# Kernel optimization log

Measured on AMD Instinct MI355X. Metric: run time of the kernel, lower is better.

Reference implementation:

```python
import jax, jax.numpy as jnp
import numpy as np

HIDDEN = 1024
STATE = 256
EXP = 4
LN_EPS = 1e-5


def setup_inputs() -> dict:
    key = jax.random.key(0)
    ks = jax.random.split(key, 10)
    B, T, H, S = 8, 2048, HIDDEN, STATE
    x = jax.random.normal(ks[0], (B, T, H), dtype=jnp.float32)
    A = jax.random.normal(ks[1], (S, S), dtype=jnp.float32) * 0.1
    Bm = jax.random.normal(ks[2], (S, H), dtype=jnp.float32) * 0.1
    C = jax.random.normal(ks[3], (H, S), dtype=jnp.float32) * 0.1
    D = jax.random.normal(ks[4], (H, H), dtype=jnp.float32) * 0.1
    ln_w = jnp.ones((H,), dtype=jnp.float32)
    ln_b = jnp.zeros((H,), dtype=jnp.float32)
    lim1 = 1.0 / np.sqrt(H)
    lim2 = 1.0 / np.sqrt(H * EXP)
    W1 = jax.random.uniform(ks[5], (H * EXP, H), minval=-lim1, maxval=lim1, dtype=jnp.float32)
    b1 = jax.random.uniform(ks[6], (H * EXP,), minval=-lim1, maxval=lim1, dtype=jnp.float32)
    W2 = jax.random.uniform(ks[7], (H, H * EXP), minval=-lim2, maxval=lim2, dtype=jnp.float32)
    b2 = jax.random.uniform(ks[8], (H,), minval=-lim2, maxval=lim2, dtype=jnp.float32)
    return {"x": x, "A": A, "Bm": Bm, "C": C, "D": D,
            "ln_w": ln_w, "ln_b": ln_b, "W1": W1, "b1": b1, "W2": W2, "b2": b2}


def _layernorm(y, w, b):
    mu = jnp.mean(y, axis=-1, keepdims=True)
    var = jnp.var(y, axis=-1, keepdims=True)
    return (y - mu) * jax.lax.rsqrt(var + LN_EPS) * w + b


def reference(x, A, Bm, C, D, ln_w, ln_b, W1, b1, W2, b2):
    Bsz, T, H = x.shape
    S = A.shape[0]
    state0 = jnp.zeros((Bsz, S), dtype=x.dtype)
    # Precompute input projections for all timesteps (big GEMMs outside the scan)
    xB = jnp.einsum('bth,sh->tbs', x, Bm)   # [T,B,S]
    xD = jnp.einsum('bth,oh->tbo', x, D)    # [T,B,H]

    def step(state, inp):
        xb_t, xd_t = inp
        state = jnp.tanh(state @ A.T + xb_t)
        out = state @ C.T + xd_t
        return state, out

    final_state, outs = jax.lax.scan(step, state0, (xB, xD))
    out_seq = jnp.transpose(outs, (1, 0, 2))  # [B,T,H]
    y = _layernorm(out_seq + x, ln_w, ln_b)
    # FFN (dropout is identity in eval mode); torch GELU default = exact erf
    h = jax.nn.gelu(jnp.einsum('bth,fh->btf', y, W1) + b1, approximate=False)
    y = y + jnp.einsum('btf,hf->bth', h, W2) + b2
    return (y, final_state)
```

## Files before the change

kernel.cpp:

```cpp
#include <hip/hip_runtime.h>
#include <math.h>

typedef unsigned short u16;
typedef unsigned int u32;

using short8 = __attribute__((ext_vector_type(8))) short;
using f32x4  = __attribute__((ext_vector_type(4))) float;
typedef _Float16 h2_t __attribute__((ext_vector_type(2)));

typedef const __attribute__((address_space(1))) unsigned int* gas_ptr;
typedef __attribute__((address_space(3))) unsigned int* las_ptr;

__device__ __forceinline__ void load_lds16(const void* g, void* l) {
    __builtin_amdgcn_global_load_lds((gas_ptr)g, (las_ptr)l, 16, 0, 0);
}

__device__ __forceinline__ u16 bf16b(float f) {
    u32 u = __builtin_bit_cast(u32, f);
    u += 0x7fffu + ((u >> 16) & 1u);
    return (u16)(u >> 16);
}
__device__ __forceinline__ float b2f(u16 h) {
    u32 u = (u32)h << 16;
    return __builtin_bit_cast(float, u);
}

__global__ void cvt_kernel(const float4* __restrict__ s, ushort4* __restrict__ d, int n4) {
    for (int i = blockIdx.x * blockDim.x + threadIdx.x; i < n4; i += gridDim.x * blockDim.x) {
        float4 v = s[i];
        ushort4 o;
        o.x = bf16b(v.x); o.y = bf16b(v.y); o.z = bf16b(v.z); o.w = bf16b(v.w);
        d[i] = o;
    }
}

template<int MODE>
__global__ __launch_bounds__(256) void gemm_bf16(
    const u16* __restrict__ Ab, const u16* __restrict__ Bb, int K, int ktiles,
    float* __restrict__ out32, u16* __restrict__ out16,
    const float* __restrict__ bias, const float* __restrict__ addf,
    const u16* __restrict__ add16, int out_stride, int out_col0)
{
    __shared__ __align__(16) u16 Als[128 * 64];
    __shared__ __align__(16) u16 Bls[128 * 64];

    const int tid  = threadIdx.x;
    const int lane = tid & 63;
    const int w    = tid >> 6;
    const int wr   = (w >> 1) * 64;
    const int wc   = (w & 1) * 64;
    const int fr   = lane & 15;
    const int fkB  = (lane >> 4) * 16;

    const size_t rb = (size_t)K * 2;
    const char* Ag = (const char*)Ab + ((size_t)blockIdx.y * 128 + (tid >> 3)) * rb + (size_t)(tid & 7) * 16;
    const char* Bg = (const char*)Bb + ((size_t)blockIdx.x * 128 + (tid >> 3)) * rb + (size_t)(tid & 7) * 16;
    char* Ald = (char*)Als + tid * 16;
    char* Bld = (char*)Bls + tid * 16;

    f32x4 acc[4][4];
#pragma unroll
    for (int m = 0; m < 4; ++m)
#pragma unroll
        for (int n = 0; n < 4; ++n)
            acc[m][n] = f32x4{0.f, 0.f, 0.f, 0.f};

    for (int kt = 0; kt < ktiles; ++kt) {
        __syncthreads();
        const char* Asrc = Ag + (size_t)kt * 128;
        const char* Bsrc = Bg + (size_t)kt * 128;
#pragma unroll
        for (int i = 0; i < 4; ++i) {
            load_lds16(Asrc + (size_t)(i * 32) * rb, Ald + i * 4096);
            load_lds16(Bsrc + (size_t)(i * 32) * rb, Bld + i * 4096);
        }
        __syncthreads();
#pragma unroll
        for (int kk = 0; kk < 2; ++kk) {
            short8 af[4], bfr[4];
#pragma unroll
            for (int m = 0; m < 4; ++m)
                af[m] = *(const short8*)((const char*)Als + (wr + m * 16 + fr) * 128 + kk * 64 + fkB);
#pragma unroll
            for (int n = 0; n < 4; ++n)
                bfr[n] = *(const short8*)((const char*)Bls + (wc + n * 16 + fr) * 128 + kk * 64 + fkB);
#pragma unroll
            for (int m = 0; m < 4; ++m)
#pragma unroll
                for (int n = 0; n < 4; ++n)
                    acc[m][n] = __builtin_amdgcn_mfma_f32_16x16x32_bf16(af[m], bfr[n], acc[m][n], 0, 0, 0);
        }
    }

    const int rbase = blockIdx.y * 128 + wr + (lane >> 4) * 4;
    const int cbase = blockIdx.x * 128 + wc + fr;
#pragma unroll
    for (int m = 0; m < 4; ++m) {
#pragma unroll
        for (int n = 0; n < 4; ++n) {
            const int col = cbase + n * 16;
#pragma unroll
            for (int r = 0; r < 4; ++r) {
                const int row = rbase + m * 16 + r;
                float v = acc[m][n][r];
                if (MODE == 0) {
                    out16[(size_t)row * out_stride + out_col0 + col] = bf16b(v);
                } else if (MODE == 1) {
                    out32[(size_t)row * 1024 + col] =
                        v + addf[(size_t)row * 1024 + col] + b2f(add16[(size_t)row * 1280 + 256 + col]);
                } else if (MODE == 2) {
                    float u = v + bias[col];
                    u = 0.5f * u * (1.0f + erff(u * 0.70710678118654752f));
                    out16[(size_t)row * out_stride + col] = bf16b(u);
                } else {
                    out32[(size_t)row * 1024 + col] =
                        v + bias[col] + b2f(add16[(size_t)row * 1024 + col]);
                }
            }
        }
    }
}

__global__ __launch_bounds__(512) void scan_kernel(
    const float* __restrict__ Am, const u16* __restrict__ xBb ,
    u16* __restrict__ states, float* __restrict__ fstate)
{
    __shared__ __align__(16) u32 stp[128];
    const int tid  = threadIdx.x;
    const int b    = blockIdx.x;
    const int s    = tid >> 1;
    const int half = tid & 1;

    h2_t a[64];
    {
        const float4* ar = (const float4*)(Am + s * 256 + half * 128);
#pragma unroll
        for (int j = 0; j < 32; ++j) {
            float4 f = ar[j];
            a[2 * j]     = h2_t{(_Float16)f.x, (_Float16)f.y};
            a[2 * j + 1] = h2_t{(_Float16)f.z, (_Float16)f.w};
        }
    }
    if (tid < 128) stp[tid] = 0u;
    const u16* xrow = xBb + (size_t)b * 2048 * 1280 + s;
    u16* srow = states + (size_t)b * 2048 * 256 + s;

    float xb0 = b2f(xrow[0]);
    float xb1 = b2f(xrow[1280]);
    float xb2 = b2f(xrow[2 * 1280]);
    float xb3 = b2f(xrow[3 * 1280]);
    __syncthreads();

#define SCAN_STEP(T, XB, NEXT)                                                      \
    {                                                                               \
        float acc = 0.f;                                                            \
        const u32* sp = stp + half * 64;                                            \
        _Pragma("unroll")                                                           \
        for (int j = 0; j < 16; ++j) {                                              \
            uint4 sv = *(const uint4*)(sp + 4 * j);                                 \
            acc = __builtin_amdgcn_fdot2(a[4 * j + 0], __builtin_bit_cast(h2_t, sv.x), acc, false); \
            acc = __builtin_amdgcn_fdot2(a[4 * j + 1], __builtin_bit_cast(h2_t, sv.y), acc, false); \
            acc = __builtin_amdgcn_fdot2(a[4 * j + 2], __builtin_bit_cast(h2_t, sv.z), acc, false); \
            acc = __builtin_amdgcn_fdot2(a[4 * j + 3], __builtin_bit_cast(h2_t, sv.w), acc, false); \
        }                                                                           \
        float z = acc + __shfl_xor(acc, 1) + (XB);                                  \
        int tp = (T) + 4 <= 2047 ? (T) + 4 : 2047;                                  \
        (XB) = b2f(xrow[(size_t)tp * 1280]);                                        \
        float e = __expf(2.f * z);                                                  \
        float h = 1.f - 2.f / (e + 1.f);                                            \
        __syncthreads();                                                            \
        if (!half) {                                                                \
            reinterpret_cast<_Float16*>(stp)[s] = (_Float16)h;                      \
            srow[(size_t)(T) * 256] = bf16b(h);                                     \
            if ((T) == 2047) fstate[b * 256 + s] = h;                               \
        }                                                                           \
        __syncthreads();                                                            \
    }

    for (int t = 0; t < 2048; t += 4) {
        SCAN_STEP(t + 0, xb0, );
        SCAN_STEP(t + 1, xb1, );
        SCAN_STEP(t + 2, xb2, );
        SCAN_STEP(t + 3, xb3, );
    }
#undef SCAN_STEP
}

__global__ __launch_bounds__(256) void ln_kernel(
    const float* __restrict__ pre , const float* __restrict__ gam,
    const float* __restrict__ bet, u16* __restrict__ ybf)
{
    const int row = blockIdx.x, tid = threadIdx.x;
    const float4 v = *(const float4*)(pre + (size_t)row * 1024 + tid * 4);
    float sum = v.x + v.y + v.z + v.w;
    float sq  = v.x * v.x + v.y * v.y + v.z * v.z + v.w * v.w;
#pragma unroll
    for (int o = 32; o; o >>= 1) { sum += __shfl_xor(sum, o); sq += __shfl_xor(sq, o); }
    __shared__ float red[8];
    const int lane = tid & 63, wv = tid >> 6;
    if (!lane) { red[wv] = sum; red[4 + wv] = sq; }
    __syncthreads();
    sum = red[0] + red[1] + red[2] + red[3];
    sq  = red[4] + red[5] + red[6] + red[7];
    const float mu  = sum * (1.f / 1024.f);
    const float var = sq * (1.f / 1024.f) - mu * mu;
    const float rs  = rsqrtf(var + 1e-5f);
    const float4 g  = *(const float4*)(gam + tid * 4);
    const float4 be = *(const float4*)(bet + tid * 4);
    ushort4 ob;
    ob.x = bf16b((v.x - mu) * rs * g.x + be.x);
    ob.y = bf16b((v.y - mu) * rs * g.y + be.y);
    ob.z = bf16b((v.z - mu) * rs * g.z + be.z);
    ob.w = bf16b((v.w - mu) * rs * g.w + be.w);
    *(ushort4*)(ybf + (size_t)row * 1024 + tid * 4) = ob;
}

extern "C" void kernel_launch(void* const* d_in, const int* in_sizes, int n_in,
                              void* d_out, int out_size, void* d_ws, size_t ws_size,
                              hipStream_t stream)
{
    const float* x    = (const float*)d_in[0];
    const float* A    = (const float*)d_in[1];
    const float* Bm   = (const float*)d_in[2];
    const float* C    = (const float*)d_in[3];
    const float* D    = (const float*)d_in[4];
    const float* ln_w = (const float*)d_in[5];
    const float* ln_b = (const float*)d_in[6];
    const float* W1   = (const float*)d_in[7];
    const float* b1   = (const float*)d_in[8];
    const float* W2   = (const float*)d_in[9];
    const float* b2   = (const float*)d_in[10];

    char* ws = (char*)d_ws;
    u16*   BmD    = (u16*)(ws + 0);
    u16*   C_bf   = (u16*)(ws + 2621440);
    u16*   W1b    = (u16*)(ws + 3145728);
    u16*   W2b    = (u16*)(ws + 11534336);
    u16*   xBD_bf = (u16*)(ws + 19922944);
    u16*   st_bf  = (u16*)(ws + 61865984);
    u16*   y_bf   = (u16*)(ws + 70254592);
    u16*   h_bf   = (u16*)(ws + 103809024);

    float* out  = (float*)d_out;
    u16*   x_bf = (u16*)d_out;

    cvt_kernel<<<2048, 256, 0, stream>>>((const float4*)x,  (ushort4*)x_bf, 4194304);
    cvt_kernel<<<256,  256, 0, stream>>>((const float4*)Bm, (ushort4*)BmD, 65536);
    cvt_kernel<<<1024, 256, 0, stream>>>((const float4*)D,  (ushort4*)(BmD + 262144), 262144);
    cvt_kernel<<<256,  256, 0, stream>>>((const float4*)C,  (ushort4*)C_bf, 65536);
    cvt_kernel<<<2048, 256, 0, stream>>>((const float4*)W1, (ushort4*)W1b, 1048576);
    cvt_kernel<<<2048, 256, 0, stream>>>((const float4*)W2, (ushort4*)W2b, 1048576);

    dim3 blk(256);
    gemm_bf16<0><<<dim3(10, 128), blk, 0, stream>>>(x_bf, BmD, 1024, 16,
        nullptr, xBD_bf, nullptr, nullptr, nullptr, 1280, 0);
    scan_kernel<<<8, 512, 0, stream>>>(A, xBD_bf, st_bf, out + 16777216);
    gemm_bf16<1><<<dim3(8, 128), blk, 0, stream>>>(st_bf, C_bf, 256, 4,
        out, nullptr, nullptr, x, xBD_bf, 1024, 0);
    ln_kernel<<<16384, 256, 0, stream>>>(out, ln_w, ln_b, y_bf);
    for (int c = 0; c < 4; ++c) {
        const u16* yc = y_bf + (size_t)c * 4096 * 1024;
        float* oc = out + (size_t)c * 4096 * 1024;
        gemm_bf16<2><<<dim3(32, 32), blk, 0, stream>>>(yc, W1b, 1024, 16,
            nullptr, h_bf, b1, nullptr, nullptr, 4096, 0);
        gemm_bf16<3><<<dim3(8, 32), blk, 0, stream>>>(h_bf, W2b, 4096, 64,
            oc, nullptr, b2, nullptr, yc, 1024, 0);
    }
}
```

Measured before the change: 2.311 ms.

## Fold D projection into state-output GEMM and widen scan to 1024 threads

```diff
diff --git a/kernel.cpp b/kernel.cpp
--- a/kernel.cpp
+++ b/kernel.cpp
@@ -33,13 +33,24 @@
         d[i] = o;
     }
 }
+__global__ void cvt_str_kernel(const float4* __restrict__ s, u16* __restrict__ d,
+                               int K4, int n4, int stride, int col0) {
+    for (int i = blockIdx.x * blockDim.x + threadIdx.x; i < n4; i += gridDim.x * blockDim.x) {
+        float4 v = s[i];
+        int r = i / K4, k4 = (i - r * K4) * 4;
+        ushort4 o;
+        o.x = bf16b(v.x); o.y = bf16b(v.y); o.z = bf16b(v.z); o.w = bf16b(v.w);
+        *(ushort4*)(d + (size_t)r * stride + col0 + k4) = o;
+    }
+}
 
 template<int MODE>
 __global__ __launch_bounds__(256) void gemm_bf16(
-    const u16* __restrict__ Ab, const u16* __restrict__ Bb, int K, int ktiles,
+    const u16* __restrict__ Ab, const u16* __restrict__ Ab2, const u16* __restrict__ Bb,
+    int K, int ktiles,
     float* __restrict__ out32, u16* __restrict__ out16,
     const float* __restrict__ bias, const float* __restrict__ addf,
-    const u16* __restrict__ add16, int out_stride, int out_col0)
+    const u16* __restrict__ add16, int out_stride)
 {
     __shared__ __align__(16) u16 Als[128 * 64];
     __shared__ __align__(16) u16 Bls[128 * 64];
@@ -52,9 +63,11 @@
     const int fr   = lane & 15;
     const int fkB  = (lane >> 4) * 16;
 
-    const size_t rb = (size_t)K * 2;
-    const char* Ag = (const char*)Ab + ((size_t)blockIdx.y * 128 + (tid >> 3)) * rb + (size_t)(tid & 7) * 16;
-    const char* Bg = (const char*)Bb + ((size_t)blockIdx.x * 128 + (tid >> 3)) * rb + (size_t)(tid & 7) * 16;
+    const size_t rbB = (size_t)K * 2;
+    const int arow = blockIdx.y * 128 + (tid >> 3);
+    const char* Ag  = (const char*)Ab + (size_t)arow * ((MODE == 1) ? 512 : rbB) + (size_t)(tid & 7) * 16;
+    const char* Ag2 = (MODE == 1) ? ((const char*)Ab2 + (size_t)arow * 2048 + (size_t)(tid & 7) * 16) : nullptr;
+    const char* Bg  = (const char*)Bb + ((size_t)blockIdx.x * 128 + (tid >> 3)) * rbB + (size_t)(tid & 7) * 16;
     char* Ald = (char*)Als + tid * 16;
     char* Bld = (char*)Bls + tid * 16;
 
@@ -67,12 +80,19 @@
 
     for (int kt = 0; kt < ktiles; ++kt) {
         __syncthreads();
-        const char* Asrc = Ag + (size_t)kt * 128;
+        const char* Asrc;
+        size_t rbA;
+        if (MODE == 1) {
+            if (kt < 4) { Asrc = Ag  + (size_t)kt * 128;       rbA = 512;  }
+            else        { Asrc = Ag2 + (size_t)(kt - 4) * 128; rbA = 2048; }
+        } else {
+            Asrc = Ag + (size_t)kt * 128; rbA = rbB;
+        }
         const char* Bsrc = Bg + (size_t)kt * 128;
 #pragma unroll
         for (int i = 0; i < 4; ++i) {
-            load_lds16(Asrc + (size_t)(i * 32) * rb, Ald + i * 4096);
-            load_lds16(Bsrc + (size_t)(i * 32) * rb, Bld + i * 4096);
+            load_lds16(Asrc + (size_t)(i * 32) * rbA, Ald + i * 4096);
+            load_lds16(Bsrc + (size_t)(i * 32) * rbB, Bld + i * 4096);
         }
         __syncthreads();
 #pragma unroll
@@ -104,10 +124,9 @@
                 const int row = rbase + m * 16 + r;
                 float v = acc[m][n][r];
                 if (MODE == 0) {
-                    out16[(size_t)row * out_stride + out_col0 + col] = bf16b(v);
+                    out16[(size_t)row * out_stride + col] = bf16b(v);
                 } else if (MODE == 1) {
-                    out32[(size_t)row * 1024 + col] =
-                        v + addf[(size_t)row * 1024 + col] + b2f(add16[(size_t)row * 1280 + 256 + col]);
+                    out16[(size_t)row * 1024 + col] = bf16b(v + addf[(size_t)row * 1024 + col]);
                 } else if (MODE == 2) {
                     float u = v + bias[col];
                     u = 0.5f * u * (1.0f + erff(u * 0.70710678118654752f));
@@ -121,56 +140,59 @@
     }
 }
 
-__global__ __launch_bounds__(512) void scan_kernel(
+__global__ __launch_bounds__(1024) void scan_kernel(
     const float* __restrict__ Am, const u16* __restrict__ xBb ,
     u16* __restrict__ states, float* __restrict__ fstate)
 {
-    __shared__ __align__(16) u32 stp[128];
-    const int tid  = threadIdx.x;
-    const int b    = blockIdx.x;
-    const int s    = tid >> 1;
-    const int half = tid & 1;
-
-    h2_t a[64];
+    __shared__ __align__(16) u32 SB[2][144];
+    const int tid = threadIdx.x;
+    const int b   = blockIdx.x;
+    const int s   = tid >> 2;
+    const int q   = tid & 3;
+
+    h2_t a[32];
     {
-        const float4* ar = (const float4*)(Am + s * 256 + half * 128);
-#pragma unroll
-        for (int j = 0; j < 32; ++j) {
+        const float4* ar = (const float4*)(Am + s * 256 + q * 64);
+#pragma unroll
+        for (int j = 0; j < 16; ++j) {
             float4 f = ar[j];
             a[2 * j]     = h2_t{(_Float16)f.x, (_Float16)f.y};
             a[2 * j + 1] = h2_t{(_Float16)f.z, (_Float16)f.w};
         }
     }
-    if (tid < 128) stp[tid] = 0u;
-    const u16* xrow = xBb + (size_t)b * 2048 * 1280 + s;
+    if (tid < 144) SB[0][tid] = 0u;
+
+    const u16* xrow = xBb + (size_t)b * 2048 * 256 + s;
     u16* srow = states + (size_t)b * 2048 * 256 + s;
+    const int widx = (s >> 6) * 72 + (s & 63);
 
     float xb0 = b2f(xrow[0]);
-    float xb1 = b2f(xrow[1280]);
-    float xb2 = b2f(xrow[2 * 1280]);
-    float xb3 = b2f(xrow[3 * 1280]);
+    float xb1 = b2f(xrow[256]);
+    float xb2 = b2f(xrow[512]);
+    float xb3 = b2f(xrow[768]);
     __syncthreads();
 
-#define SCAN_STEP(T, XB, NEXT)                                                      \
+#define SCAN_STEP(T, XB)                                                            \
     {                                                                               \
-        float acc = 0.f;                                                            \
-        const u32* sp = stp + half * 64;                                            \
+        const u32* sp = SB[(T) & 1] + q * 36;                                       \
+        float ac0 = 0.f, ac1 = 0.f, ac2 = 0.f, ac3 = 0.f;                           \
         _Pragma("unroll")                                                           \
-        for (int j = 0; j < 16; ++j) {                                              \
+        for (int j = 0; j < 8; ++j) {                                               \
             uint4 sv = *(const uint4*)(sp + 4 * j);                                 \
-            acc = __builtin_amdgcn_fdot2(a[4 * j + 0], __builtin_bit_cast(h2_t, sv.x), acc, false); \
-            acc = __builtin_amdgcn_fdot2(a[4 * j + 1], __builtin_bit_cast(h2_t, sv.y), acc, false); \
-            acc = __builtin_amdgcn_fdot2(a[4 * j + 2], __builtin_bit_cast(h2_t, sv.z), acc, false); \
-            acc = __builtin_amdgcn_fdot2(a[4 * j + 3], __builtin_bit_cast(h2_t, sv.w), acc, false); \
+            ac0 = __builtin_amdgcn_fdot2(a[4 * j + 0], __builtin_bit_cast(h2_t, sv.x), ac0, false); \
+            ac1 = __builtin_amdgcn_fdot2(a[4 * j + 1], __builtin_bit_cast(h2_t, sv.y), ac1, false); \
+            ac2 = __builtin_amdgcn_fdot2(a[4 * j + 2], __builtin_bit_cast(h2_t, sv.z), ac2, false); \
+            ac3 = __builtin_amdgcn_fdot2(a[4 * j + 3], __builtin_bit_cast(h2_t, sv.w), ac3, false); \
         }                                                                           \
-        float z = acc + __shfl_xor(acc, 1) + (XB);                                  \
+        float zq = (ac0 + ac1) + (ac2 + ac3);                                       \
+        zq += __shfl_xor(zq, 1);                                                    \
+        float z = zq + __shfl_xor(zq, 2) + (XB);                                    \
         int tp = (T) + 4 <= 2047 ? (T) + 4 : 2047;                                  \
-        (XB) = b2f(xrow[(size_t)tp * 1280]);                                        \
+        (XB) = b2f(xrow[(size_t)tp * 256]);                                        \
         float e = __expf(2.f * z);                                                  \
         float h = 1.f - 2.f / (e + 1.f);                                            \
-        __syncthreads();                                                            \
-        if (!half) {                                                                \
-            reinterpret_cast<_Float16*>(stp)[s] = (_Float16)h;                      \
+        if (!q) {                                                                   \
+            reinterpret_cast<_Float16*>(SB[((T) + 1) & 1])[widx] = (_Float16)h;     \
             srow[(size_t)(T) * 256] = bf16b(h);                                     \
             if ((T) == 2047) fstate[b * 256 + s] = h;                               \
         }                                                                           \
@@ -178,22 +200,23 @@
     }
 
     for (int t = 0; t < 2048; t += 4) {
-        SCAN_STEP(t + 0, xb0, );
-        SCAN_STEP(t + 1, xb1, );
-        SCAN_STEP(t + 2, xb2, );
-        SCAN_STEP(t + 3, xb3, );
+        SCAN_STEP(t + 0, xb0);
+        SCAN_STEP(t + 1, xb1);
+        SCAN_STEP(t + 2, xb2);
+        SCAN_STEP(t + 3, xb3);
     }
 #undef SCAN_STEP
 }
 
 __global__ __launch_bounds__(256) void ln_kernel(
-    const float* __restrict__ pre , const float* __restrict__ gam,
+    const u16* __restrict__ pre , const float* __restrict__ gam,
     const float* __restrict__ bet, u16* __restrict__ ybf)
 {
     const int row = blockIdx.x, tid = threadIdx.x;
-    const float4 v = *(const float4*)(pre + (size_t)row * 1024 + tid * 4);
-    float sum = v.x + v.y + v.z + v.w;
-    float sq  = v.x * v.x + v.y * v.y + v.z * v.z + v.w * v.w;
+    const ushort4 pv = *(const ushort4*)(pre + (size_t)row * 1024 + tid * 4);
+    float vx = b2f(pv.x), vy = b2f(pv.y), vz = b2f(pv.z), vw = b2f(pv.w);
+    float sum = vx + vy + vz + vw;
+    float sq  = vx * vx + vy * vy + vz * vz + vw * vw;
 #pragma unroll
     for (int o = 32; o; o >>= 1) { sum += __shfl_xor(sum, o); sq += __shfl_xor(sq, o); }
     __shared__ float red[8];
@@ -208,10 +231,10 @@
     const float4 g  = *(const float4*)(gam + tid * 4);
     const float4 be = *(const float4*)(bet + tid * 4);
     ushort4 ob;
-    ob.x = bf16b((v.x - mu) * rs * g.x + be.x);
-    ob.y = bf16b((v.y - mu) * rs * g.y + be.y);
-    ob.z = bf16b((v.z - mu) * rs * g.z + be.z);
-    ob.w = bf16b((v.w - mu) * rs * g.w + be.w);
+    ob.x = bf16b((vx - mu) * rs * g.x + be.x);
+    ob.y = bf16b((vy - mu) * rs * g.y + be.y);
+    ob.z = bf16b((vz - mu) * rs * g.z + be.z);
+    ob.w = bf16b((vw - mu) * rs * g.w + be.w);
     *(ushort4*)(ybf + (size_t)row * 1024 + tid * 4) = ob;
 }
 
@@ -232,38 +255,38 @@
     const float* b2   = (const float*)d_in[10];
 
     char* ws = (char*)d_ws;
-    u16*   BmD    = (u16*)(ws + 0);
-    u16*   C_bf   = (u16*)(ws + 2621440);
-    u16*   W1b    = (u16*)(ws + 3145728);
-    u16*   W2b    = (u16*)(ws + 11534336);
-    u16*   xBD_bf = (u16*)(ws + 19922944);
-    u16*   st_bf  = (u16*)(ws + 61865984);
-    u16*   y_bf   = (u16*)(ws + 70254592);
-    u16*   h_bf   = (u16*)(ws + 103809024);
-
-    float* out  = (float*)d_out;
-    u16*   x_bf = (u16*)d_out;
-
-    cvt_kernel<<<2048, 256, 0, stream>>>((const float4*)x,  (ushort4*)x_bf, 4194304);
-    cvt_kernel<<<256,  256, 0, stream>>>((const float4*)Bm, (ushort4*)BmD, 65536);
-    cvt_kernel<<<1024, 256, 0, stream>>>((const float4*)D,  (ushort4*)(BmD + 262144), 262144);
-    cvt_kernel<<<256,  256, 0, stream>>>((const float4*)C,  (ushort4*)C_bf, 65536);
+    u16* Bm_bf  = (u16*)(ws + 0);
+    u16* CD_bf  = (u16*)(ws + 524288);
+    u16* W1b    = (u16*)(ws + 3145728);
+    u16* W2b    = (u16*)(ws + 11534336);
+    u16* xB_bf  = (u16*)(ws + 19922944);
+    u16* st_bf  = (u16*)(ws + 28311552);
+    u16* y_bf   = (u16*)(ws + 36700160);
+    u16* pre_bf = (u16*)(ws + 70254592);
+    u16* xh_bf  = (u16*)(ws + 103809024);
+
+    float* out = (float*)d_out;
+
+    cvt_kernel<<<2048, 256, 0, stream>>>((const float4*)x,  (ushort4*)xh_bf, 4194304);
+    cvt_kernel<<<256,  256, 0, stream>>>((const float4*)Bm, (ushort4*)Bm_bf, 65536);
+    cvt_str_kernel<<<256,  256, 0, stream>>>((const float4*)C, CD_bf, 64, 65536, 1280, 0);
+    cvt_str_kernel<<<1024, 256, 0, stream>>>((const float4*)D, CD_bf, 256, 262144, 1280, 256);
     cvt_kernel<<<2048, 256, 0, stream>>>((const float4*)W1, (ushort4*)W1b, 1048576);
     cvt_kernel<<<2048, 256, 0, stream>>>((const float4*)W2, (ushort4*)W2b, 1048576);
 
     dim3 blk(256);
-    gemm_bf16<0><<<dim3(10, 128), blk, 0, stream>>>(x_bf, BmD, 1024, 16,
-        nullptr, xBD_bf, nullptr, nullptr, nullptr, 1280, 0);
-    scan_kernel<<<8, 512, 0, stream>>>(A, xBD_bf, st_bf, out + 16777216);
-    gemm_bf16<1><<<dim3(8, 128), blk, 0, stream>>>(st_bf, C_bf, 256, 4,
-        out, nullptr, nullptr, x, xBD_bf, 1024, 0);
-    ln_kernel<<<16384, 256, 0, stream>>>(out, ln_w, ln_b, y_bf);
+    gemm_bf16<0><<<dim3(2, 128), blk, 0, stream>>>(xh_bf, nullptr, Bm_bf, 1024, 16,
+        nullptr, xB_bf, nullptr, nullptr, nullptr, 256);
+    scan_kernel<<<8, 1024, 0, stream>>>(A, xB_bf, st_bf, out + 16777216);
+    gemm_bf16<1><<<dim3(8, 128), blk, 0, stream>>>(st_bf, xh_bf, CD_bf, 1280, 20,
+        nullptr, pre_bf, nullptr, x, nullptr, 1024);
+    ln_kernel<<<16384, 256, 0, stream>>>(pre_bf, ln_w, ln_b, y_bf);
     for (int c = 0; c < 4; ++c) {
         const u16* yc = y_bf + (size_t)c * 4096 * 1024;
         float* oc = out + (size_t)c * 4096 * 1024;
-        gemm_bf16<2><<<dim3(32, 32), blk, 0, stream>>>(yc, W1b, 1024, 16,
-            nullptr, h_bf, b1, nullptr, nullptr, 4096, 0);
-        gemm_bf16<3><<<dim3(8, 32), blk, 0, stream>>>(h_bf, W2b, 4096, 64,
-            oc, nullptr, b2, nullptr, yc, 1024, 0);
-    }
-}
+        gemm_bf16<2><<<dim3(32, 32), blk, 0, stream>>>(yc, nullptr, W1b, 1024, 16,
+            nullptr, xh_bf, b1, nullptr, nullptr, 4096);
+        gemm_bf16<3><<<dim3(8, 32), blk, 0, stream>>>(xh_bf, nullptr, W2b, 4096, 64,
+            oc, nullptr, b2, nullptr, yc, 1024);
+    }
+}
```

After: 2.221 ms. -3.9%, faster.
